# Kernel optimization log

Hardware: AMD Instinct MI355X
Metric: run time of the kernel (lower is better)

The kernel has to match this reference:

```python
import jax, jax.numpy as jnp
import numpy as np

N, L, H, D_HEAD, P = 2, 1024, 8, 64, 1
DIM = H * D_HEAD


def setup_inputs() -> dict:
    key0 = jax.random.key(0)
    ks = jax.random.split(key0, 7)
    query = jax.random.normal(ks[0], (N, L, DIM), dtype=jnp.float32)
    key = jax.random.normal(ks[1], (N, L, DIM), dtype=jnp.float32)
    scale = 1.0 / np.sqrt(DIM)
    Wq = jax.random.normal(ks[2], (DIM, DIM), dtype=jnp.float32) * scale
    Wk = jax.random.normal(ks[3], (DIM, DIM), dtype=jnp.float32) * scale
    Wv = jax.random.normal(ks[4], (DIM, DIM), dtype=jnp.float32) * scale
    position_weight = jax.random.uniform(ks[5], (H, P, D_HEAD), dtype=jnp.float32) * 2 - 1
    position_bias = jax.random.uniform(ks[6], (H, D_HEAD), dtype=jnp.float32) * 2 - 1
    return {"query": query, "key": key, "Wq": Wq, "Wk": Wk, "Wv": Wv,
            "position_weight": position_weight, "position_bias": position_bias}


def _kernel_fn(x):
    # _log_exp_kernel: positive feature map log(1 + exp(x)) (softplus)
    return jax.nn.softplus(x)


def _causal_term(qf, kf, v):
    """Linear-complexity causal attention term.
    qf, kf: (N,H,L,d) feature-mapped query/key; v: (N,H,L,d) values.
    Returns numerator (N,H,L,d) and denominator (N,H,L)."""
    # cumulative key-value outer products: (N,H,L,d,d)
    kv = jnp.cumsum(jnp.einsum('nhkd,nhke->nhkde', kf, v), axis=2)
    num = jnp.einsum('nhqd,nhqde->nhqe', qf, kv)
    den = jnp.einsum('nhqd,nhqd->nhq', qf, jnp.cumsum(kf, axis=2))
    return num, den


def reference(query, key, Wq, Wk, Wv, position_weight, position_bias):
    n, lq, dim = query.shape
    lk = key.shape[1]
    h, p, d = position_weight.shape
    kernel = _kernel_fn
    # projections (torch Linear: x @ W.T), reshape to heads, transpose to (N,H,L,d)
    q = kernel((query @ Wq.T).reshape(n, lq, h, d)).transpose(0, 2, 1, 3)
    k = kernel((key @ Wk.T).reshape(n, lk, h, d)).transpose(0, 2, 1, 3)
    v = ((key @ Wv.T).reshape(n, lk, h, d)).transpose(0, 2, 1, 3)
    # default positions: arange, expanded to (N,L,P)
    qpos = jnp.broadcast_to(jnp.arange(lq, dtype=query.dtype)[None, :, None], (n, lq, p))
    kpos = jnp.broadcast_to(jnp.arange(lk, dtype=key.dtype)[None, :, None], (n, lk, p))
    pq = jnp.einsum('nlp,hpd->nhld', qpos, position_weight) \
         + jax.nn.sigmoid(position_bias)[None, :, None, :] * jnp.pi
    pk = jnp.einsum('nlp,hpd->nhld', kpos, position_weight)
    # three branches: cos, sin, plain (trig identity split of cos(pq - pk) RPE)
    num_c, den_c = _causal_term(q * jnp.cos(pq), k * jnp.cos(pk), v)
    num_s, den_s = _causal_term(q * jnp.sin(pq), k * jnp.sin(pk), v)
    num_p, den_p = _causal_term(q, k, v)
    num = num_c + num_s + num_p
    den = den_c + den_s + den_p
    attention = num / den[..., None]  # scaled=True
    return attention.transpose(0, 2, 1, 3).reshape(n, lq, dim)
```

## Files before the change

kernel.cpp:

```cpp
#include <hip/hip_runtime.h>
#include <hip/hip_bf16.h>

#define LSEQ   1024
#define NHEAD  8
#define DH     64
#define DIM    512
#define CHUNK  64
#define NCHUNK 16
#define NHTOT  16
#define PAD    68
#define LDB    68
#define LDA    72

typedef __attribute__((ext_vector_type(8))) short short8;
typedef __attribute__((ext_vector_type(4))) float floatx4;

__device__ __forceinline__ float softplusf_(float x) {
    if (x > 20.f) return x;
    return log1pf(expf(x));
}
__device__ __forceinline__ unsigned short bf16_rne(float x) {
    unsigned int u = __float_as_uint(x);
    u += 0x7FFFu + ((u >> 16) & 1u);
    return (unsigned short)(u >> 16);
}
__device__ __forceinline__ float bf16_tof(unsigned short h) {
    return __uint_as_float(((unsigned int)h) << 16);
}

__global__ __launch_bounds__(256) void proj_kernel(
    const float* __restrict__ query, const float* __restrict__ key,
    const float* __restrict__ Wq, const float* __restrict__ Wk,
    const float* __restrict__ Wv,
    float* __restrict__ qbuf, float* __restrict__ kbuf, float* __restrict__ vbuf)
{
    const int mt  = blockIdx.x;
    const int ot  = blockIdx.y;
    const int sel = blockIdx.z;
    const int t   = threadIdx.x;

    const float* __restrict__ X = (sel == 0) ? query : key;
    const float* __restrict__ W = (sel == 0) ? Wq : (sel == 1) ? Wk : Wv;
    float* __restrict__ obuf = (sel == 0) ? qbuf : (sel == 1) ? kbuf : vbuf;

    __shared__ unsigned short As[64 * LDB];
    __shared__ unsigned short Bs[64 * LDB];

    const int m0 = mt * 64, o0 = ot * 64;
    const int lane = t & 63, wave = t >> 6;
    const int quad = lane >> 4, l16 = lane & 15;
    const int wm = wave >> 1, wn = wave & 1;

    const int srow = t >> 2;
    const int sc16 = (t & 3) * 16;

    floatx4 acc[2][2];
    #pragma unroll
    for (int i = 0; i < 2; ++i)
        #pragma unroll
        for (int j = 0; j < 2; ++j) acc[i][j] = (floatx4){0.f, 0.f, 0.f, 0.f};

    float4 ax[4], bx4[4];
    #pragma unroll
    for (int i = 0; i < 4; ++i) {
        ax[i]  = *(const float4*)&X[(size_t)(m0 + srow) * DIM + sc16 + i * 4];
        bx4[i] = *(const float4*)&W[(size_t)(o0 + srow) * DIM + sc16 + i * 4];
    }

    for (int kt = 0; kt < DIM; kt += 64) {
        __syncthreads();
        {
            short8 a0, a1, b0, b1;
            #pragma unroll
            for (int i = 0; i < 2; ++i) {
                const float va[4] = {ax[i].x, ax[i].y, ax[i].z, ax[i].w};
                const float vb[4] = {bx4[i].x, bx4[i].y, bx4[i].z, bx4[i].w};
                #pragma unroll
                for (int j = 0; j < 4; ++j) {
                    a0[i * 4 + j] = (short)bf16_rne(va[j]);
                    b0[i * 4 + j] = (short)bf16_rne(vb[j]);
                }
            }
            #pragma unroll
            for (int i = 2; i < 4; ++i) {
                const float va[4] = {ax[i].x, ax[i].y, ax[i].z, ax[i].w};
                const float vb[4] = {bx4[i].x, bx4[i].y, bx4[i].z, bx4[i].w};
                #pragma unroll
                for (int j = 0; j < 4; ++j) {
                    a1[(i - 2) * 4 + j] = (short)bf16_rne(va[j]);
                    b1[(i - 2) * 4 + j] = (short)bf16_rne(vb[j]);
                }
            }
            *(short8*)&As[srow * LDB + sc16]     = a0;
            *(short8*)&As[srow * LDB + sc16 + 8] = a1;
            *(short8*)&Bs[srow * LDB + sc16]     = b0;
            *(short8*)&Bs[srow * LDB + sc16 + 8] = b1;
        }
        __syncthreads();

        if (kt + 64 < DIM) {
            #pragma unroll
            for (int i = 0; i < 4; ++i) {
                ax[i]  = *(const float4*)&X[(size_t)(m0 + srow) * DIM + kt + 64 + sc16 + i * 4];
                bx4[i] = *(const float4*)&W[(size_t)(o0 + srow) * DIM + kt + 64 + sc16 + i * 4];
            }
        }

        #pragma unroll
        for (int s = 0; s < 2; ++s) {
            short8 af[2], bf[2];
            #pragma unroll
            for (int mi = 0; mi < 2; ++mi)
                af[mi] = *(const short8*)&As[(wm * 32 + mi * 16 + l16) * LDB + s * 32 + quad * 8];
            #pragma unroll
            for (int ni = 0; ni < 2; ++ni)
                bf[ni] = *(const short8*)&Bs[(wn * 32 + ni * 16 + l16) * LDB + s * 32 + quad * 8];
            #pragma unroll
            for (int ni = 0; ni < 2; ++ni)
                #pragma unroll
                for (int mi = 0; mi < 2; ++mi)
                    acc[mi][ni] = __builtin_amdgcn_mfma_f32_16x16x32_bf16(af[mi], bf[ni], acc[mi][ni], 0, 0, 0);
        }
    }

    const int h = ot;
    #pragma unroll
    for (int mi = 0; mi < 2; ++mi)
        #pragma unroll
        for (int ni = 0; ni < 2; ++ni) {
            const int d = wn * 32 + ni * 16 + l16;
            #pragma unroll
            for (int r = 0; r < 4; ++r) {
                const int m = m0 + wm * 32 + mi * 16 + quad * 4 + r;
                const int n = m >> 10, l = m & (LSEQ - 1);
                float val = acc[mi][ni][r];
                if (sel < 2) val = softplusf_(val);
                obuf[(((size_t)(n * NHEAD + h)) * LSEQ + l) * DH + d] = val;
            }
        }
}

__global__ __launch_bounds__(256) void chunksum_kernel(
    const float* __restrict__ kbuf, const float* __restrict__ vbuf,
    const float* __restrict__ pw,
    float* __restrict__ Ssum, float* __restrict__ zsum)
{
    const int c  = blockIdx.x;
    const int nh = blockIdx.y;
    const int br = blockIdx.z;
    const int h  = nh & (NHEAD - 1);
    const int t  = threadIdx.x;

    __shared__ float kf[CHUNK][PAD];
    __shared__ float vt[CHUNK][PAD];

    const size_t base = ((size_t)nh * LSEQ + (size_t)c * CHUNK) * DH;

    #pragma unroll
    for (int i = 0; i < 4; ++i) {
        const int e4 = i * 256 + t;
        const int k  = e4 >> 4;
        const int c4 = (e4 & 15) * 4;
        const float4 kv = *(const float4*)&kbuf[base + (size_t)k * DH + c4];
        const float4 vv = *(const float4*)&vbuf[base + (size_t)k * DH + c4];
        const float4 wv = *(const float4*)&pw[h * DH + c4];
        const float pos = (float)(c * CHUNK + k);
        float4 f;
        if (br == 0)      { f.x = 1.f; f.y = 1.f; f.z = 1.f; f.w = 1.f; }
        else if (br == 1) { f.x = cosf(pos * wv.x); f.y = cosf(pos * wv.y);
                            f.z = cosf(pos * wv.z); f.w = cosf(pos * wv.w); }
        else              { f.x = sinf(pos * wv.x); f.y = sinf(pos * wv.y);
                            f.z = sinf(pos * wv.z); f.w = sinf(pos * wv.w); }
        float4 ko;
        ko.x = kv.x * f.x; ko.y = kv.y * f.y; ko.z = kv.z * f.z; ko.w = kv.w * f.w;
        *(float4*)&kf[k][c4] = ko;
        *(float4*)&vt[k][c4] = vv;
    }
    __syncthreads();

    const int d0 = (t >> 4) * 4;
    const int e0 = (t & 15) * 4;

    float S[4][4] = {};
    float zr[4] = {};
    #pragma unroll 4
    for (int k = 0; k < CHUNK; ++k) {
        const float4 rv = *(const float4*)&vt[k][d0];
        const float4 cv = *(const float4*)&kf[k][e0];
        S[0][0] += rv.x * cv.x; S[0][1] += rv.x * cv.y;
        S[0][2] += rv.x * cv.z; S[0][3] += rv.x * cv.w;
        S[1][0] += rv.y * cv.x; S[1][1] += rv.y * cv.y;
        S[1][2] += rv.y * cv.z; S[1][3] += rv.y * cv.w;
        S[2][0] += rv.z * cv.x; S[2][1] += rv.z * cv.y;
        S[2][2] += rv.z * cv.z; S[2][3] += rv.z * cv.w;
        S[3][0] += rv.w * cv.x; S[3][1] += rv.w * cv.y;
        S[3][2] += rv.w * cv.z; S[3][3] += rv.w * cv.w;
        zr[0] += cv.x; zr[1] += cv.y; zr[2] += cv.z; zr[3] += cv.w;
    }

    float* Sg = Ssum + ((size_t)(br * NHTOT + nh) * NCHUNK + c) * (DH * DH);
    #pragma unroll
    for (int i = 0; i < 4; ++i) {
        float4 o;
        o.x = S[i][0]; o.y = S[i][1]; o.z = S[i][2]; o.w = S[i][3];
        *(float4*)&Sg[(d0 + i) * DH + e0] = o;
    }
    if ((t >> 4) == 0) {
        float* zg = zsum + ((size_t)(br * NHTOT + nh) * NCHUNK + c) * DH;
        #pragma unroll
        for (int i = 0; i < 4; ++i) zg[e0 + i] = zr[i];
    }
}

__global__ __launch_bounds__(256) void scan_kernel(
    float* __restrict__ Ssum, float* __restrict__ zsum)
{
    const int b = blockIdx.x;
    const int s = blockIdx.y;
    const int idx = s * 256 + threadIdx.x;

    float* S = Ssum + (size_t)b * NCHUNK * (DH * DH);
    float v[NCHUNK];
    #pragma unroll
    for (int c = 0; c < NCHUNK; ++c) v[c] = S[c * (DH * DH) + idx];
    float run = 0.f;
    #pragma unroll
    for (int c = 0; c < NCHUNK; ++c) {
        const float nv = v[c];
        S[c * (DH * DH) + idx] = run;
        run += nv;
    }
    if (s == 0 && threadIdx.x < DH) {
        float* z = zsum + (size_t)b * NCHUNK * DH;
        float zv[NCHUNK];
        #pragma unroll
        for (int c = 0; c < NCHUNK; ++c) zv[c] = z[c * DH + threadIdx.x];
        float zr = 0.f;
        #pragma unroll
        for (int c = 0; c < NCHUNK; ++c) {
            const float nv = zv[c];
            z[c * DH + threadIdx.x] = zr;
            zr += nv;
        }
    }
}

__global__ __launch_bounds__(256) void attn_kernel(
    const float* __restrict__ qbuf, const float* __restrict__ kbuf,
    const float* __restrict__ vbuf,
    const float* __restrict__ Ssum, const float* __restrict__ zsum,
    const float* __restrict__ pw, const float* __restrict__ pb,
    float* __restrict__ numP, float* __restrict__ denP)
{
    const int c  = blockIdx.x;
    const int nh = blockIdx.y;
    const int br = blockIdx.z;
    const int n  = nh >> 3;
    const int h  = nh & (NHEAD - 1);
    const int t  = threadIdx.x;
    const int lane = t & 63, wave = t >> 6;
    const int quad = lane >> 4, l16 = lane & 15;
    const int wm = wave >> 1, wn = wave & 1;

    __shared__ unsigned short qfL[64 * LDA];
    __shared__ unsigned short kfL[64 * LDA];
    __shared__ unsigned short vTL[64 * LDA];
    __shared__ unsigned short SpL[64 * LDA];
    __shared__ unsigned short scA[64 * LDA];
    __shared__ float zl[DH];
    __shared__ float dpart[8][64];

    const size_t base = ((size_t)nh * LSEQ + (size_t)c * CHUNK) * DH;
    const float* Sg = Ssum + ((size_t)(br * NHTOT + nh) * NCHUNK + c) * (DH * DH);
    const float PI_ = 3.14159265358979323846f;

    #pragma unroll
    for (int i = 0; i < 4; ++i) {
        const int idx = i * 256 + t;
        const int r  = idx >> 4;
        const int c4 = (idx & 15) * 4;
        const float4 qv = *(const float4*)&qbuf[base + (size_t)r * DH + c4];
        const float4 kv = *(const float4*)&kbuf[base + (size_t)r * DH + c4];
        const float4 vv = *(const float4*)&vbuf[base + (size_t)r * DH + c4];
        const float4 sv = *(const float4*)&Sg[r * DH + c4];
        float tq[4] = {1.f, 1.f, 1.f, 1.f}, tk[4] = {1.f, 1.f, 1.f, 1.f};
        if (br != 0) {
            const float4 wv  = *(const float4*)&pw[h * DH + c4];
            const float4 pbv = *(const float4*)&pb[h * DH + c4];
            const float w4[4] = {wv.x, wv.y, wv.z, wv.w};
            const float b4[4] = {pbv.x, pbv.y, pbv.z, pbv.w};
            const float pos = (float)(c * CHUNK + r);
            #pragma unroll
            for (int j = 0; j < 4; ++j) {
                const float bias = PI_ / (1.f + expf(-b4[j]));
                if (br == 1) { tq[j] = cosf(pos * w4[j] + bias); tk[j] = cosf(pos * w4[j]); }
                else         { tq[j] = sinf(pos * w4[j] + bias); tk[j] = sinf(pos * w4[j]); }
            }
        }
        const float q4[4] = {qv.x, qv.y, qv.z, qv.w};
        const float k4[4] = {kv.x, kv.y, kv.z, kv.w};
        const float v4[4] = {vv.x, vv.y, vv.z, vv.w};
        const float s4[4] = {sv.x, sv.y, sv.z, sv.w};
        ushort4 qh, kh, sh;
        unsigned short* pq = (unsigned short*)&qh;
        unsigned short* pk = (unsigned short*)&kh;
        unsigned short* ps = (unsigned short*)&sh;
        #pragma unroll
        for (int j = 0; j < 4; ++j) {
            pq[j] = bf16_rne(q4[j] * tq[j]);
            pk[j] = bf16_rne(k4[j] * tk[j]);
            ps[j] = bf16_rne(s4[j]);
            vTL[(c4 + j) * LDA + r] = bf16_rne(v4[j]);
        }
        *(ushort4*)&qfL[r * LDA + c4] = qh;
        *(ushort4*)&kfL[r * LDA + c4] = kh;
        *(ushort4*)&SpL[r * LDA + c4] = sh;
    }
    if (t < DH)
        zl[t] = zsum[((size_t)(br * NHTOT + nh) * NCHUNK + c) * DH + t];
    __syncthreads();

    floatx4 acc1[2][2], acc2[2][2];
    #pragma unroll
    for (int i = 0; i < 2; ++i)
        #pragma unroll
        for (int j = 0; j < 2; ++j) {
            acc1[i][j] = (floatx4){0.f, 0.f, 0.f, 0.f};
            acc2[i][j] = (floatx4){0.f, 0.f, 0.f, 0.f};
        }
    #pragma unroll
    for (int kk = 0; kk < 2; ++kk) {
        short8 a[2], b1[2], b2[2];
        #pragma unroll
        for (int mi = 0; mi < 2; ++mi)
            a[mi] = *(const short8*)&qfL[(wm * 32 + mi * 16 + l16) * LDA + kk * 32 + quad * 8];
        #pragma unroll
        for (int ni = 0; ni < 2; ++ni) {
            b1[ni] = *(const short8*)&kfL[(wn * 32 + ni * 16 + l16) * LDA + kk * 32 + quad * 8];
            b2[ni] = *(const short8*)&SpL[(wn * 32 + ni * 16 + l16) * LDA + kk * 32 + quad * 8];
        }
        #pragma unroll
        for (int ni = 0; ni < 2; ++ni)
            #pragma unroll
            for (int mi = 0; mi < 2; ++mi) {
                acc1[mi][ni] = __builtin_amdgcn_mfma_f32_16x16x32_bf16(a[mi], b1[ni], acc1[mi][ni], 0, 0, 0);
                acc2[mi][ni] = __builtin_amdgcn_mfma_f32_16x16x32_bf16(a[mi], b2[ni], acc2[mi][ni], 0, 0, 0);
            }
    }

    {
        const int l = t & 63, seg = t >> 6;
        float s = 0.f;
        #pragma unroll
        for (int j2 = 0; j2 < 2; ++j2) {
            const short8 v8 = *(const short8*)&qfL[l * LDA + seg * 16 + j2 * 8];
            #pragma unroll
            for (int j = 0; j < 8; ++j)
                s += bf16_tof((unsigned short)v8[j]) * zl[seg * 16 + j2 * 8 + j];
        }
        dpart[seg][l] = s;
    }

    #pragma unroll
    for (int mi = 0; mi < 2; ++mi)
        #pragma unroll
        for (int ni = 0; ni < 2; ++ni) {
            const int kcol = wn * 32 + ni * 16 + l16;
            #pragma unroll
            for (int r = 0; r < 4; ++r) {
                const int lrow = wm * 32 + mi * 16 + quad * 4 + r;
                const float v = (kcol <= lrow) ? acc1[mi][ni][r] : 0.f;
                scA[lrow * LDA + kcol] = bf16_rne(v);
            }
        }
    __syncthreads();

    #pragma unroll
    for (int kk = 0; kk < 2; ++kk) {
        short8 a[2], b[2];
        #pragma unroll
        for (int mi = 0; mi < 2; ++mi)
            a[mi] = *(const short8*)&scA[(wm * 32 + mi * 16 + l16) * LDA + kk * 32 + quad * 8];
        #pragma unroll
        for (int ni = 0; ni < 2; ++ni)
            b[ni] = *(const short8*)&vTL[(wn * 32 + ni * 16 + l16) * LDA + kk * 32 + quad * 8];
        #pragma unroll
        for (int ni = 0; ni < 2; ++ni)
            #pragma unroll
            for (int mi = 0; mi < 2; ++mi)
                acc2[mi][ni] = __builtin_amdgcn_mfma_f32_16x16x32_bf16(a[mi], b[ni], acc2[mi][ni], 0, 0, 0);
    }

    {
        const int l = t & 63, seg = t >> 6;
        float s = 0.f;
        #pragma unroll
        for (int j2 = 0; j2 < 2; ++j2) {
            const short8 v8 = *(const short8*)&scA[l * LDA + seg * 16 + j2 * 8];
            #pragma unroll
            for (int j = 0; j < 8; ++j) s += bf16_tof((unsigned short)v8[j]);
        }
        dpart[4 + seg][l] = s;
    }
    __syncthreads();

    if (t < DH) {
        const float dl = dpart[0][t] + dpart[1][t] + dpart[2][t] + dpart[3][t]
                       + dpart[4][t] + dpart[5][t] + dpart[6][t] + dpart[7][t];
        denP[((size_t)(br * NHTOT + nh)) * LSEQ + c * CHUNK + t] = dl;
    }

    #pragma unroll
    for (int mi = 0; mi < 2; ++mi)
        #pragma unroll
        for (int ni = 0; ni < 2; ++ni) {
            const int e = wn * 32 + ni * 16 + l16;
            #pragma unroll
            for (int r = 0; r < 4; ++r) {
                const int l = c * CHUNK + wm * 32 + mi * 16 + quad * 4 + r;
                numP[(((size_t)br * 2 + n) * LSEQ + l) * DIM + h * DH + e] = acc2[mi][ni][r];
            }
        }
}

__global__ __launch_bounds__(256) void combine_kernel(
    const float* __restrict__ numP, const float* __restrict__ denP,
    float* __restrict__ outp)
{
    const int i = blockIdx.x * 256 + threadIdx.x;
    const int row = i >> 7;
    const int ci  = i & 127;
    const int n = row >> 10, l = row & (LSEQ - 1), h = ci >> 4;
    const int nh = n * NHEAD + h;
    const float4* N = (const float4*)numP;
    const float4 a = N[i];
    const float4 b = N[i + 262144];
    const float4 cc = N[i + 524288];
    const float ds = denP[(size_t)nh * LSEQ + l]
                   + denP[((size_t)NHTOT + nh) * LSEQ + l]
                   + denP[((size_t)2 * NHTOT + nh) * LSEQ + l];
    const float inv = 1.f / ds;
    float4 o;
    o.x = (a.x + b.x + cc.x) * inv;
    o.y = (a.y + b.y + cc.y) * inv;
    o.z = (a.z + b.z + cc.z) * inv;
    o.w = (a.w + b.w + cc.w) * inv;
    ((float4*)outp)[i] = o;
}

extern "C" void kernel_launch(void* const* d_in, const int* in_sizes, int n_in,
                              void* d_out, int out_size, void* d_ws, size_t ws_size,
                              hipStream_t stream) {
    const float* query = (const float*)d_in[0];
    const float* key   = (const float*)d_in[1];
    const float* Wq    = (const float*)d_in[2];
    const float* Wk    = (const float*)d_in[3];
    const float* Wv    = (const float*)d_in[4];
    const float* pw    = (const float*)d_in[5];
    const float* pb    = (const float*)d_in[6];

    float* F = (float*)d_ws;
    float* qbuf = F;
    float* kbuf = F + 1048576;
    float* vbuf = F + 2097152;
    float* Ssum = F + 3145728;
    float* zsum = F + 6291456;
    float* numP = F + 6340608;
    float* denP = F + 9486336;

    proj_kernel<<<dim3(32, 8, 3), 256, 0, stream>>>(
        query, key, Wq, Wk, Wv, qbuf, kbuf, vbuf);
    chunksum_kernel<<<dim3(NCHUNK, NHTOT, 3), 256, 0, stream>>>(
        kbuf, vbuf, pw, Ssum, zsum);
    scan_kernel<<<dim3(3 * NHTOT, NCHUNK), 256, 0, stream>>>(Ssum, zsum);
    attn_kernel<<<dim3(NCHUNK, NHTOT, 3), 256, 0, stream>>>(
        qbuf, kbuf, vbuf, Ssum, zsum, pw, pb, numP, denP);
    combine_kernel<<<dim3(1024), 256, 0, stream>>>(numP, denP, (float*)d_out);
}
```

Before: 123.7 us.

## Store projections in bf16, use MFMA for chunk sums, fold scan into attention

The projection kernel now writes q/k/v as bf16 instead of fp32, which halves intermediate traffic. The chunk-sum kernel computes the per-chunk K^T V state with bf16 MFMA instead of scalar FP32 FMAs. The separate scan kernel is removed: each attention block sums all earlier chunk states itself, which saves a launch and a read/write pass. In exchange, later chunks read up to 15 earlier 64x64 states (redundant reads that grow with chunk index, so load is uneven across blocks), and the bf16 rounding happens earlier, which costs some precision.

After: 132.0 us. +6.7%, slower.

```diff
diff --git a/kernel.cpp b/kernel.cpp
--- a/kernel.cpp
+++ b/kernel.cpp
@@ -8,7 +8,6 @@
 #define CHUNK  64
 #define NCHUNK 16
 #define NHTOT  16
-#define PAD    68
 #define LDB    68
 #define LDA    72
 
@@ -32,7 +31,8 @@
     const float* __restrict__ query, const float* __restrict__ key,
     const float* __restrict__ Wq, const float* __restrict__ Wk,
     const float* __restrict__ Wv,
-    float* __restrict__ qbuf, float* __restrict__ kbuf, float* __restrict__ vbuf)
+    unsigned short* __restrict__ qbuf, unsigned short* __restrict__ kbuf,
+    unsigned short* __restrict__ vbuf)
 {
     const int mt  = blockIdx.x;
     const int ot  = blockIdx.y;
@@ -41,7 +41,7 @@
 
     const float* __restrict__ X = (sel == 0) ? query : key;
     const float* __restrict__ W = (sel == 0) ? Wq : (sel == 1) ? Wk : Wv;
-    float* __restrict__ obuf = (sel == 0) ? qbuf : (sel == 1) ? kbuf : vbuf;
+    unsigned short* __restrict__ obuf = (sel == 0) ? qbuf : (sel == 1) ? kbuf : vbuf;
 
     __shared__ unsigned short As[64 * LDB];
     __shared__ unsigned short Bs[64 * LDB];
@@ -135,13 +135,13 @@
                 const int n = m >> 10, l = m & (LSEQ - 1);
                 float val = acc[mi][ni][r];
                 if (sel < 2) val = softplusf_(val);
-                obuf[(((size_t)(n * NHEAD + h)) * LSEQ + l) * DH + d] = val;
+                obuf[(((size_t)(n * NHEAD + h)) * LSEQ + l) * DH + d] = bf16_rne(val);
             }
         }
 }
 
 __global__ __launch_bounds__(256) void chunksum_kernel(
-    const float* __restrict__ kbuf, const float* __restrict__ vbuf,
+    const unsigned short* __restrict__ kbuf, const unsigned short* __restrict__ vbuf,
     const float* __restrict__ pw,
     float* __restrict__ Ssum, float* __restrict__ zsum)
 {
@@ -150,104 +150,99 @@
     const int br = blockIdx.z;
     const int h  = nh & (NHEAD - 1);
     const int t  = threadIdx.x;
-
-    __shared__ float kf[CHUNK][PAD];
-    __shared__ float vt[CHUNK][PAD];
+    const int lane = t & 63, wave = t >> 6;
+    const int quad = lane >> 4, l16 = lane & 15;
+    const int wm = wave >> 1, wn = wave & 1;
+
+    __shared__ unsigned short kfT[64 * LDA];
+    __shared__ unsigned short vT[64 * LDA];
+    __shared__ float dpart[4][64];
 
     const size_t base = ((size_t)nh * LSEQ + (size_t)c * CHUNK) * DH;
 
     #pragma unroll
     for (int i = 0; i < 4; ++i) {
-        const int e4 = i * 256 + t;
-        const int k  = e4 >> 4;
-        const int c4 = (e4 & 15) * 4;
-        const float4 kv = *(const float4*)&kbuf[base + (size_t)k * DH + c4];
-        const float4 vv = *(const float4*)&vbuf[base + (size_t)k * DH + c4];
-        const float4 wv = *(const float4*)&pw[h * DH + c4];
-        const float pos = (float)(c * CHUNK + k);
-        float4 f;
-        if (br == 0)      { f.x = 1.f; f.y = 1.f; f.z = 1.f; f.w = 1.f; }
-        else if (br == 1) { f.x = cosf(pos * wv.x); f.y = cosf(pos * wv.y);
-                            f.z = cosf(pos * wv.z); f.w = cosf(pos * wv.w); }
-        else              { f.x = sinf(pos * wv.x); f.y = sinf(pos * wv.y);
-                            f.z = sinf(pos * wv.z); f.w = sinf(pos * wv.w); }
-        float4 ko;
-        ko.x = kv.x * f.x; ko.y = kv.y * f.y; ko.z = kv.z * f.z; ko.w = kv.w * f.w;
-        *(float4*)&kf[k][c4] = ko;
-        *(float4*)&vt[k][c4] = vv;
+        const int idx = i * 256 + t;
+        const int r  = idx >> 4;
+        const int c4 = (idx & 15) * 4;
+        const ushort4 kv = *(const ushort4*)&kbuf[base + (size_t)r * DH + c4];
+        const ushort4 vv = *(const ushort4*)&vbuf[base + (size_t)r * DH + c4];
+        const unsigned short* pk = (const unsigned short*)&kv;
+        const unsigned short* pv = (const unsigned short*)&vv;
+        float tk[4] = {1.f, 1.f, 1.f, 1.f};
+        if (br != 0) {
+            const float4 wv = *(const float4*)&pw[h * DH + c4];
+            const float w4[4] = {wv.x, wv.y, wv.z, wv.w};
+            const float pos = (float)(c * CHUNK + r);
+            #pragma unroll
+            for (int j = 0; j < 4; ++j)
+                tk[j] = (br == 1) ? cosf(pos * w4[j]) : sinf(pos * w4[j]);
+        }
+        #pragma unroll
+        for (int j = 0; j < 4; ++j) {
+            kfT[(c4 + j) * LDA + r] = (br == 0) ? pk[j]
+                                     : bf16_rne(bf16_tof(pk[j]) * tk[j]);
+            vT[(c4 + j) * LDA + r] = pv[j];
+        }
     }
     __syncthreads();
 
-    const int d0 = (t >> 4) * 4;
-    const int e0 = (t & 15) * 4;
-
-    float S[4][4] = {};
-    float zr[4] = {};
-    #pragma unroll 4
-    for (int k = 0; k < CHUNK; ++k) {
-        const float4 rv = *(const float4*)&vt[k][d0];
-        const float4 cv = *(const float4*)&kf[k][e0];
-        S[0][0] += rv.x * cv.x; S[0][1] += rv.x * cv.y;
-        S[0][2] += rv.x * cv.z; S[0][3] += rv.x * cv.w;
-        S[1][0] += rv.y * cv.x; S[1][1] += rv.y * cv.y;
-        S[1][2] += rv.y * cv.z; S[1][3] += rv.y * cv.w;
-        S[2][0] += rv.z * cv.x; S[2][1] += rv.z * cv.y;
-        S[2][2] += rv.z * cv.z; S[2][3] += rv.z * cv.w;
-        S[3][0] += rv.w * cv.x; S[3][1] += rv.w * cv.y;
-        S[3][2] += rv.w * cv.z; S[3][3] += rv.w * cv.w;
-        zr[0] += cv.x; zr[1] += cv.y; zr[2] += cv.z; zr[3] += cv.w;
+    floatx4 acc[2][2];
+    #pragma unroll
+    for (int i = 0; i < 2; ++i)
+        #pragma unroll
+        for (int j = 0; j < 2; ++j) acc[i][j] = (floatx4){0.f, 0.f, 0.f, 0.f};
+
+    #pragma unroll
+    for (int kk = 0; kk < 2; ++kk) {
+        short8 a[2], b[2];
+        #pragma unroll
+        for (int mi = 0; mi < 2; ++mi)
+            a[mi] = *(const short8*)&vT[(wm * 32 + mi * 16 + l16) * LDA + kk * 32 + quad * 8];
+        #pragma unroll
+        for (int ni = 0; ni < 2; ++ni)
+            b[ni] = *(const short8*)&kfT[(wn * 32 + ni * 16 + l16) * LDA + kk * 32 + quad * 8];
+        #pragma unroll
+        for (int ni = 0; ni < 2; ++ni)
+            #pragma unroll
+            for (int mi = 0; mi < 2; ++mi)
+                acc[mi][ni] = __builtin_amdgcn_mfma_f32_16x16x32_bf16(a[mi], b[ni], acc[mi][ni], 0, 0, 0);
+    }
+
+    {
+        const int d = t & 63, seg = t >> 6;
+        float s = 0.f;
+        #pragma unroll
+        for (int j2 = 0; j2 < 2; ++j2) {
+            const short8 v8 = *(const short8*)&kfT[d * LDA + seg * 16 + j2 * 8];
+            #pragma unroll
+            for (int j = 0; j < 8; ++j) s += bf16_tof((unsigned short)v8[j]);
+        }
+        dpart[seg][d] = s;
+    }
+    __syncthreads();
+    if (t < DH) {
+        zsum[((size_t)(br * NHTOT + nh) * NCHUNK + c) * DH + t] =
+            dpart[0][t] + dpart[1][t] + dpart[2][t] + dpart[3][t];
     }
 
     float* Sg = Ssum + ((size_t)(br * NHTOT + nh) * NCHUNK + c) * (DH * DH);
     #pragma unroll
-    for (int i = 0; i < 4; ++i) {
-        float4 o;
-        o.x = S[i][0]; o.y = S[i][1]; o.z = S[i][2]; o.w = S[i][3];
-        *(float4*)&Sg[(d0 + i) * DH + e0] = o;
-    }
-    if ((t >> 4) == 0) {
-        float* zg = zsum + ((size_t)(br * NHTOT + nh) * NCHUNK + c) * DH;
-        #pragma unroll
-        for (int i = 0; i < 4; ++i) zg[e0 + i] = zr[i];
-    }
-}
-
-__global__ __launch_bounds__(256) void scan_kernel(
-    float* __restrict__ Ssum, float* __restrict__ zsum)
-{
-    const int b = blockIdx.x;
-    const int s = blockIdx.y;
-    const int idx = s * 256 + threadIdx.x;
-
-    float* S = Ssum + (size_t)b * NCHUNK * (DH * DH);
-    float v[NCHUNK];
-    #pragma unroll
-    for (int c = 0; c < NCHUNK; ++c) v[c] = S[c * (DH * DH) + idx];
-    float run = 0.f;
-    #pragma unroll
-    for (int c = 0; c < NCHUNK; ++c) {
-        const float nv = v[c];
-        S[c * (DH * DH) + idx] = run;
-        run += nv;
-    }
-    if (s == 0 && threadIdx.x < DH) {
-        float* z = zsum + (size_t)b * NCHUNK * DH;
-        float zv[NCHUNK];
-        #pragma unroll
-        for (int c = 0; c < NCHUNK; ++c) zv[c] = z[c * DH + threadIdx.x];
-        float zr = 0.f;
-        #pragma unroll
-        for (int c = 0; c < NCHUNK; ++c) {
-            const float nv = zv[c];
-            z[c * DH + threadIdx.x] = zr;
-            zr += nv;
-        }
-    }
+    for (int mi = 0; mi < 2; ++mi)
+        #pragma unroll
+        for (int ni = 0; ni < 2; ++ni) {
+            const int d = wn * 32 + ni * 16 + l16;
+            #pragma unroll
+            for (int r = 0; r < 4; ++r) {
+                const int e = wm * 32 + mi * 16 + quad * 4 + r;
+                Sg[e * DH + d] = acc[mi][ni][r];
+            }
+        }
 }
 
 __global__ __launch_bounds__(256) void attn_kernel(
-    const float* __restrict__ qbuf, const float* __restrict__ kbuf,
-    const float* __restrict__ vbuf,
+    const unsigned short* __restrict__ qbuf, const unsigned short* __restrict__ kbuf,
+    const unsigned short* __restrict__ vbuf,
     const float* __restrict__ Ssum, const float* __restrict__ zsum,
     const float* __restrict__ pw, const float* __restrict__ pb,
     float* __restrict__ numP, float* __restrict__ denP)
@@ -271,20 +266,55 @@
     __shared__ float dpart[8][64];
 
     const size_t base = ((size_t)nh * LSEQ + (size_t)c * CHUNK) * DH;
-    const float* Sg = Ssum + ((size_t)(br * NHTOT + nh) * NCHUNK + c) * (DH * DH);
     const float PI_ = 3.14159265358979323846f;
 
+    int rr[4], cc4[4];
     #pragma unroll
     for (int i = 0; i < 4; ++i) {
         const int idx = i * 256 + t;
-        const int r  = idx >> 4;
-        const int c4 = (idx & 15) * 4;
-        const float4 qv = *(const float4*)&qbuf[base + (size_t)r * DH + c4];
-        const float4 kv = *(const float4*)&kbuf[base + (size_t)r * DH + c4];
-        const float4 vv = *(const float4*)&vbuf[base + (size_t)r * DH + c4];
-        const float4 sv = *(const float4*)&Sg[r * DH + c4];
-        float tq[4] = {1.f, 1.f, 1.f, 1.f}, tk[4] = {1.f, 1.f, 1.f, 1.f};
-        if (br != 0) {
+        rr[i]  = idx >> 4;
+        cc4[i] = (idx & 15) * 4;
+    }
+    float sacc[16];
+    #pragma unroll
+    for (int j = 0; j < 16; ++j) sacc[j] = 0.f;
+    {
+        const float* Sg0 = Ssum + (size_t)(br * NHTOT + nh) * NCHUNK * (DH * DH);
+        for (int cp = 0; cp < c; ++cp) {
+            const float* Sgc = Sg0 + (size_t)cp * (DH * DH);
+            #pragma unroll
+            for (int i = 0; i < 4; ++i) {
+                const float4 sv = *(const float4*)&Sgc[rr[i] * DH + cc4[i]];
+                sacc[i * 4 + 0] += sv.x; sacc[i * 4 + 1] += sv.y;
+                sacc[i * 4 + 2] += sv.z; sacc[i * 4 + 3] += sv.w;
+            }
+        }
+    }
+    if (t < DH) {
+        float zacc = 0.f;
+        const float* zg = zsum + (size_t)(br * NHTOT + nh) * NCHUNK * DH;
+        for (int cp = 0; cp < c; ++cp) zacc += zg[cp * DH + t];
+        zl[t] = zacc;
+    }
+
+    #pragma unroll
+    for (int i = 0; i < 4; ++i) {
+        const int r  = rr[i];
+        const int c4 = cc4[i];
+        const ushort4 qv = *(const ushort4*)&qbuf[base + (size_t)r * DH + c4];
+        const ushort4 kv = *(const ushort4*)&kbuf[base + (size_t)r * DH + c4];
+        const ushort4 vv = *(const ushort4*)&vbuf[base + (size_t)r * DH + c4];
+        const unsigned short* pq0 = (const unsigned short*)&qv;
+        const unsigned short* pk0 = (const unsigned short*)&kv;
+        const unsigned short* pv0 = (const unsigned short*)&vv;
+        ushort4 qh, kh, sh;
+        unsigned short* pq = (unsigned short*)&qh;
+        unsigned short* pk = (unsigned short*)&kh;
+        unsigned short* ps = (unsigned short*)&sh;
+        if (br == 0) {
+            #pragma unroll
+            for (int j = 0; j < 4; ++j) { pq[j] = pq0[j]; pk[j] = pk0[j]; }
+        } else {
             const float4 wv  = *(const float4*)&pw[h * DH + c4];
             const float4 pbv = *(const float4*)&pb[h * DH + c4];
             const float w4[4] = {wv.x, wv.y, wv.z, wv.w};
@@ -293,31 +323,22 @@
             #pragma unroll
             for (int j = 0; j < 4; ++j) {
                 const float bias = PI_ / (1.f + expf(-b4[j]));
-                if (br == 1) { tq[j] = cosf(pos * w4[j] + bias); tk[j] = cosf(pos * w4[j]); }
-                else         { tq[j] = sinf(pos * w4[j] + bias); tk[j] = sinf(pos * w4[j]); }
-            }
-        }
-        const float q4[4] = {qv.x, qv.y, qv.z, qv.w};
-        const float k4[4] = {kv.x, kv.y, kv.z, kv.w};
-        const float v4[4] = {vv.x, vv.y, vv.z, vv.w};
-        const float s4[4] = {sv.x, sv.y, sv.z, sv.w};
-        ushort4 qh, kh, sh;
-        unsigned short* pq = (unsigned short*)&qh;
-        unsigned short* pk = (unsigned short*)&kh;
-        unsigned short* ps = (unsigned short*)&sh;
+                float tq, tk;
+                if (br == 1) { tq = cosf(pos * w4[j] + bias); tk = cosf(pos * w4[j]); }
+                else         { tq = sinf(pos * w4[j] + bias); tk = sinf(pos * w4[j]); }
+                pq[j] = bf16_rne(bf16_tof(pq0[j]) * tq);
+                pk[j] = bf16_rne(bf16_tof(pk0[j]) * tk);
+            }
+        }
         #pragma unroll
         for (int j = 0; j < 4; ++j) {
-            pq[j] = bf16_rne(q4[j] * tq[j]);
-            pk[j] = bf16_rne(k4[j] * tk[j]);
-            ps[j] = bf16_rne(s4[j]);
-            vTL[(c4 + j) * LDA + r] = bf16_rne(v4[j]);
+            ps[j] = bf16_rne(sacc[i * 4 + j]);
+            vTL[(c4 + j) * LDA + r] = pv0[j];
         }
         *(ushort4*)&qfL[r * LDA + c4] = qh;
         *(ushort4*)&kfL[r * LDA + c4] = kh;
         *(ushort4*)&SpL[r * LDA + c4] = sh;
     }
-    if (t < DH)
-        zl[t] = zsum[((size_t)(br * NHTOT + nh) * NCHUNK + c) * DH + t];
     __syncthreads();
 
     floatx4 acc1[2][2], acc2[2][2];
@@ -459,20 +480,20 @@
     const float* pw    = (const float*)d_in[5];
     const float* pb    = (const float*)d_in[6];
 
+    unsigned short* U = (unsigned short*)d_ws;
     float* F = (float*)d_ws;
-    float* qbuf = F;
-    float* kbuf = F + 1048576;
-    float* vbuf = F + 2097152;
-    float* Ssum = F + 3145728;
-    float* zsum = F + 6291456;
-    float* numP = F + 6340608;
-    float* denP = F + 9486336;
+    unsigned short* qbuf = U;
+    unsigned short* kbuf = U + 1048576;
+    unsigned short* vbuf = U + 2097152;
+    float* Ssum = F + 1572864;
+    float* zsum = F + 4718592;
+    float* numP = F + 4767744;
+    float* denP = F + 7913472;
 
     proj_kernel<<<dim3(32, 8, 3), 256, 0, stream>>>(
         query, key, Wq, Wk, Wv, qbuf, kbuf, vbuf);
     chunksum_kernel<<<dim3(NCHUNK, NHTOT, 3), 256, 0, stream>>>(
         kbuf, vbuf, pw, Ssum, zsum);
-    scan_kernel<<<dim3(3 * NHTOT, NCHUNK), 256, 0, stream>>>(Ssum, zsum);
     attn_kernel<<<dim3(NCHUNK, NHTOT, 3), 256, 0, stream>>>(
         qbuf, kbuf, vbuf, Ssum, zsum, pw, pb, numP, denP);
     combine_kernel<<<dim3(1024), 256, 0, stream>>>(numP, denP, (float*)d_out);
```
